# Kernel optimization log

Hardware: AMD Instinct MI355X
Metric: run time of the kernel (lower is better)

Reference implementation:

```python
import jax, jax.numpy as jnp
import numpy as np

B, N, H, OUT, T = 8192, 82, 10, 5, 3  # batch, n_nodes, hidden, output_channel, time_step


def setup_inputs() -> dict:
    key = jax.random.key(0)
    ks = jax.random.split(key, 20)

    def lin(kw, kb, fin, fout):
        w = jax.random.normal(kw, (fout, fin), jnp.float32) * (1.0 / np.sqrt(fin))
        b = jax.random.normal(kb, (fout,), jnp.float32) * 0.01
        return w, b

    w3w, b3w = lin(ks[0], ks[1], 2 * H, H)
    w3u, b3u = lin(ks[2], ks[3], H, H)
    w4w, b4w = lin(ks[4], ks[5], 2 * H, H)
    w5w, b5w = lin(ks[6], ks[7], 2 * H, H)
    w5u, b5u = lin(ks[8], ks[9], H, H)
    wout, bout = lin(ks[10], ks[11], 2 * H, OUT)
    return {
        'x': jax.random.normal(ks[12], (B, N, H), jnp.float32),
        'in_adj': jax.random.uniform(ks[13], (N, N), jnp.float32),
        'out_adj': jax.random.uniform(ks[14], (N, N), jnp.float32),
        'w3w': w3w, 'b3w': b3w, 'w3u': w3u, 'b3u': b3u,
        'w4w': w4w, 'b4w': b4w, 'w5w': w5w, 'b5w': b5w,
        'w5u': w5u, 'b5u': b5u, 'wout': wout, 'bout': bout,
    }


def _dense(v, w, b):
    return v @ w.T + b


def reference(x, in_adj, out_adj, w3w, b3w, w3u, b3u, w4w, b4w,
              w5w, b5w, w5u, b5u, wout, bout):
    b, n, h = x.shape
    nodes = x  # [B, N, H]
    fn = nodes.reshape(b * n, h)
    for _ in range(T):
        # neighbor aggregation; adjacency shared across batch (torch tiles it with repeat)
        a_in = jnp.einsum('ij,bjh->bih', in_adj, nodes)
        a_out = jnp.einsum('ij,bjh->bih', out_adj, nodes)
        av = jnp.concatenate([a_in, a_out], axis=-1).reshape(b * n, 2 * h)
        fn = nodes.reshape(b * n, h)
        zv = jax.nn.sigmoid(_dense(av, w3w, b3w) + _dense(fn, w3u, b3u))
        # NOTE: original torch code (bug) reuses fc_eq3_u here instead of fc_eq4_u
        rv = jax.nn.sigmoid(_dense(av, w4w, b4w) + _dense(fn, w3u, b3u))
        hv = jnp.tanh(_dense(av, w5w, b5w) + _dense(rv * fn, w5u, b5u))
        fn = (1.0 - zv) * fn + zv * hv
        nodes = fn.reshape(b, n, h)
    out_in = jnp.concatenate([fn, x.reshape(b * n, h)], axis=1)
    output = jnp.tanh(_dense(out_in, wout, bout))
    return output, fn
```

## Files before the change

kernel.cpp:

```cpp
#include <hip/hip_runtime.h>
#include <math.h>

#define B_TOTAL 8192
#define NN      82
#define HH      10
#define OUTC    5
#define TSTEP   3
#define BPB     3
#define THREADS 256
#define ROWP    12

__device__ __forceinline__ float sigmoid_(float x) {
    return 1.0f / (1.0f + __expf(-x));
}
__device__ __forceinline__ float tanh_(float x) {
    float e = __expf(2.0f * x);
    return 1.0f - 2.0f / (e + 1.0f);
}

__global__ void transpose_adj_kernel(const float* __restrict__ in_adj,
                                     const float* __restrict__ out_adj,
                                     float* __restrict__ adjT) {
    int idx = blockIdx.x * blockDim.x + threadIdx.x;
    if (idx < NN * NN) {
        int i = idx / NN;
        int j = idx - i * NN;
        adjT[j * NN + i]           = in_adj[i * NN + j];
        adjT[NN * NN + j * NN + i] = out_adj[i * NN + j];
    }
}

extern "C" __global__ __launch_bounds__(THREADS)
void ggnn_kernel(const float* __restrict__ x,
                 const float* __restrict__ adjT,
                 const float* __restrict__ w3w, const float* __restrict__ b3w,
                 const float* __restrict__ w3u, const float* __restrict__ b3u,
                 const float* __restrict__ w4w, const float* __restrict__ b4w,
                 const float* __restrict__ w5w, const float* __restrict__ b5w,
                 const float* __restrict__ w5u, const float* __restrict__ b5u,
                 const float* __restrict__ wout, const float* __restrict__ bout,
                 float* __restrict__ out0, float* __restrict__ out_fn)
{
    __shared__ __align__(16) float nodes[BPB][NN][ROWP];

    const int t     = threadIdx.x;
    const int bbase = blockIdx.x * BPB;
    const int bl    = t / NN;
    const int node  = t - bl * NN;
    const bool active = (bl < BPB) && (bbase + bl < B_TOTAL);
    const int b = bbase + bl;

    {
        int nb    = min(BPB, B_TOTAL - bbase);
        int nelem = nb * NN * HH;
        const float* src = x + (size_t)bbase * NN * HH;
        float* dst = &nodes[0][0][0];
        for (int k = t; k < nelem; k += THREADS) {
            int row = k / HH;
            int col = k - row * HH;
            dst[row * ROWP + col] = src[k];
        }
    }
    __syncthreads();

    float fn[HH];
    if (active) {
        #pragma unroll
        for (int h = 0; h < HH; ++h) fn[h] = nodes[bl][node][h];
    }

    const float* adjT_in  = adjT;
    const float* adjT_out = adjT + NN * NN;

    for (int step = 0; step < TSTEP; ++step) {
        float ai[HH], ao[HH];
        if (active) {
            #pragma unroll
            for (int h = 0; h < HH; ++h) { ai[h] = 0.0f; ao[h] = 0.0f; }

            const float* nrow = &nodes[bl][0][0];
            #pragma unroll 4
            for (int j = 0; j < NN; ++j) {
                float win = adjT_in [j * NN + node];
                float wot = adjT_out[j * NN + node];
                const float4* nj4 = reinterpret_cast<const float4*>(nrow + j * ROWP);
                float4 v0 = nj4[0];
                float4 v1 = nj4[1];
                float2 v2 = *reinterpret_cast<const float2*>(nrow + j * ROWP + 8);
                float v[HH] = {v0.x, v0.y, v0.z, v0.w, v1.x, v1.y, v1.z, v1.w, v2.x, v2.y};
                #pragma unroll
                for (int h = 0; h < HH; ++h) {
                    ai[h] = fmaf(win, v[h], ai[h]);
                    ao[h] = fmaf(wot, v[h], ao[h]);
                }
            }

            float av[2 * HH];
            #pragma unroll
            for (int h = 0; h < HH; ++h) { av[h] = ai[h]; av[HH + h] = ao[h]; }

            float u3[HH];
            #pragma unroll
            for (int h = 0; h < HH; ++h) {
                float s = b3u[h];
                #pragma unroll
                for (int k = 0; k < HH; ++k) s = fmaf(w3u[h * HH + k], fn[k], s);
                u3[h] = s;
            }

            float zv[HH], rv[HH];
            #pragma unroll
            for (int h = 0; h < HH; ++h) {
                float s1 = b3w[h];
                float s2 = b4w[h];
                #pragma unroll
                for (int k = 0; k < 2 * HH; ++k) {
                    s1 = fmaf(w3w[h * 2 * HH + k], av[k], s1);
                    s2 = fmaf(w4w[h * 2 * HH + k], av[k], s2);
                }
                zv[h] = sigmoid_(s1 + u3[h]);
                rv[h] = sigmoid_(s2 + u3[h]);
            }

            float rf[HH];
            #pragma unroll
            for (int k = 0; k < HH; ++k) rf[k] = rv[k] * fn[k];

            float hv[HH];
            #pragma unroll
            for (int h = 0; h < HH; ++h) {
                float s = b5w[h] + b5u[h];
                #pragma unroll
                for (int k = 0; k < 2 * HH; ++k) s = fmaf(w5w[h * 2 * HH + k], av[k], s);
                #pragma unroll
                for (int k = 0; k < HH; ++k)     s = fmaf(w5u[h * HH + k], rf[k], s);
                hv[h] = tanh_(s);
            }

            #pragma unroll
            for (int h = 0; h < HH; ++h) fn[h] = fn[h] + zv[h] * (hv[h] - fn[h]);
        }

        __syncthreads();
        if (active) {
            #pragma unroll
            for (int h = 0; h < HH; ++h) nodes[bl][node][h] = fn[h];
        }
        __syncthreads();
    }

    if (active) {
        size_t row = (size_t)b * NN + node;
        const float* xr = x + row * HH;
        float xi[HH];
        #pragma unroll
        for (int h = 0; h < HH; ++h) xi[h] = xr[h];

        #pragma unroll
        for (int c = 0; c < OUTC; ++c) {
            float s = bout[c];
            #pragma unroll
            for (int k = 0; k < HH; ++k) s = fmaf(wout[c * 2 * HH + k],      fn[k], s);
            #pragma unroll
            for (int k = 0; k < HH; ++k) s = fmaf(wout[c * 2 * HH + HH + k], xi[k], s);
            out0[row * OUTC + c] = tanh_(s);
        }
        #pragma unroll
        for (int h = 0; h < HH; ++h) out_fn[row * HH + h] = fn[h];
    }
}

extern "C" void kernel_launch(void* const* d_in, const int* in_sizes, int n_in,
                              void* d_out, int out_size, void* d_ws, size_t ws_size,
                              hipStream_t stream) {
    const float* x       = (const float*)d_in[0];
    const float* in_adj  = (const float*)d_in[1];
    const float* out_adj = (const float*)d_in[2];
    const float* w3w = (const float*)d_in[3];
    const float* b3w = (const float*)d_in[4];
    const float* w3u = (const float*)d_in[5];
    const float* b3u = (const float*)d_in[6];
    const float* w4w = (const float*)d_in[7];
    const float* b4w = (const float*)d_in[8];
    const float* w5w = (const float*)d_in[9];
    const float* b5w = (const float*)d_in[10];
    const float* w5u = (const float*)d_in[11];
    const float* b5u = (const float*)d_in[12];
    const float* wout = (const float*)d_in[13];
    const float* bout = (const float*)d_in[14];

    float* adjT = (float*)d_ws;
    float* out0 = (float*)d_out;
    float* out_fn = out0 + (size_t)B_TOTAL * NN * OUTC;

    transpose_adj_kernel<<<(NN * NN + 255) / 256, 256, 0, stream>>>(in_adj, out_adj, adjT);

    int grid = (B_TOTAL + BPB - 1) / BPB;
    ggnn_kernel<<<grid, THREADS, 0, stream>>>(
        x, adjT, w3w, b3w, w3u, b3u, w4w, b4w, w5w, b5w, w5u, b5u,
        wout, bout, out0, out_fn);
}
```

Measured before the change: 275.8 us.

## Process two batches per thread and interleave in/out adjacency as float2

Each thread now handles one node for two batch elements (6 batches per block instead of 3), so each adjacency weight loaded from global memory is reused across two batches. The in/out adjacency matrices are packed into a single interleaved float2 array, so one load fetches both weights. This halves the grid size and adjacency traffic per batch, but roughly doubles per-thread register pressure, which can reduce occupancy. Shared memory per block also doubles.

```diff
diff --git a/kernel.cpp b/kernel.cpp
--- a/kernel.cpp
+++ b/kernel.cpp
@@ -6,7 +6,9 @@
 #define HH      10
 #define OUTC    5
 #define TSTEP   3
-#define BPB     3
+#define GRP     3
+#define BPT     2
+#define BPB     (GRP * BPT)
 #define THREADS 256
 #define ROWP    12
 
@@ -20,19 +22,69 @@
 
 __global__ void transpose_adj_kernel(const float* __restrict__ in_adj,
                                      const float* __restrict__ out_adj,
-                                     float* __restrict__ adjT) {
+                                     float2* __restrict__ adjI) {
     int idx = blockIdx.x * blockDim.x + threadIdx.x;
     if (idx < NN * NN) {
         int i = idx / NN;
         int j = idx - i * NN;
-        adjT[j * NN + i]           = in_adj[i * NN + j];
-        adjT[NN * NN + j * NN + i] = out_adj[i * NN + j];
+        adjI[j * NN + i] = make_float2(in_adj[idx], out_adj[idx]);
+    }
+}
+
+__device__ __forceinline__ void gru_update(
+    float fn[HH], const float ai[HH], const float ao[HH],
+    const float* __restrict__ w3w, const float* __restrict__ b3w,
+    const float* __restrict__ w3u, const float* __restrict__ b3u,
+    const float* __restrict__ w4w, const float* __restrict__ b4w,
+    const float* __restrict__ w5w, const float* __restrict__ b5w,
+    const float* __restrict__ w5u, const float* __restrict__ b5u)
+{
+    float u3[HH];
+    #pragma unroll
+    for (int h = 0; h < HH; ++h) {
+        float s = b3u[h];
+        #pragma unroll
+        for (int k = 0; k < HH; ++k) s = fmaf(w3u[h * HH + k], fn[k], s);
+        u3[h] = s;
+    }
+
+    float zv[HH], rv[HH];
+    #pragma unroll
+    for (int h = 0; h < HH; ++h) {
+        float s1 = b3w[h];
+        float s2 = b4w[h];
+        #pragma unroll
+        for (int k = 0; k < HH; ++k) {
+            s1 = fmaf(w3w[h * 2 * HH + k],      ai[k], s1);
+            s1 = fmaf(w3w[h * 2 * HH + HH + k], ao[k], s1);
+            s2 = fmaf(w4w[h * 2 * HH + k],      ai[k], s2);
+            s2 = fmaf(w4w[h * 2 * HH + HH + k], ao[k], s2);
+        }
+        zv[h] = sigmoid_(s1 + u3[h]);
+        rv[h] = sigmoid_(s2 + u3[h]);
+    }
+
+    float rf[HH];
+    #pragma unroll
+    for (int k = 0; k < HH; ++k) rf[k] = rv[k] * fn[k];
+
+    #pragma unroll
+    for (int h = 0; h < HH; ++h) {
+        float s = b5w[h] + b5u[h];
+        #pragma unroll
+        for (int k = 0; k < HH; ++k) {
+            s = fmaf(w5w[h * 2 * HH + k],      ai[k], s);
+            s = fmaf(w5w[h * 2 * HH + HH + k], ao[k], s);
+            s = fmaf(w5u[h * HH + k],          rf[k], s);
+        }
+        float hv = tanh_(s);
+        fn[h] = fn[h] + zv[h] * (hv - fn[h]);
     }
 }
 
 extern "C" __global__ __launch_bounds__(THREADS)
 void ggnn_kernel(const float* __restrict__ x,
-                 const float* __restrict__ adjT,
+                 const float2* __restrict__ adjI,
                  const float* __restrict__ w3w, const float* __restrict__ b3w,
                  const float* __restrict__ w3u, const float* __restrict__ b3u,
                  const float* __restrict__ w4w, const float* __restrict__ b4w,
@@ -47,15 +99,18 @@
     const int bbase = blockIdx.x * BPB;
     const int bl    = t / NN;
     const int node  = t - bl * NN;
-    const bool active = (bl < BPB) && (bbase + bl < B_TOTAL);
-    const int b = bbase + bl;
+    const bool grp_ok = (bl < GRP);
+    const int b0 = bbase + bl;
+    const int b1 = bbase + bl + GRP;
+    const bool a0 = grp_ok && (b0 < B_TOTAL);
+    const bool a1 = grp_ok && (b1 < B_TOTAL);
 
     {
-        int nb    = min(BPB, B_TOTAL - bbase);
-        int nelem = nb * NN * HH;
-        const float* src = x + (size_t)bbase * NN * HH;
+        const size_t gbase = (size_t)bbase * NN * HH;
+        const int    limit = (int)min((size_t)(BPB * NN * HH), (size_t)B_TOTAL * NN * HH - gbase);
+        const float* src = x + gbase;
         float* dst = &nodes[0][0][0];
-        for (int k = t; k < nelem; k += THREADS) {
+        for (int k = t; k < limit; k += THREADS) {
             int row = k / HH;
             int col = k - row * HH;
             dst[row * ROWP + col] = src[k];
@@ -63,93 +118,69 @@
     }
     __syncthreads();
 
-    float fn[HH];
-    if (active) {
-        #pragma unroll
-        for (int h = 0; h < HH; ++h) fn[h] = nodes[bl][node][h];
-    }
-
-    const float* adjT_in  = adjT;
-    const float* adjT_out = adjT + NN * NN;
+    float fn0[HH], fn1[HH];
+    if (grp_ok) {
+        #pragma unroll
+        for (int h = 0; h < HH; ++h) {
+            fn0[h] = nodes[bl][node][h];
+            fn1[h] = nodes[bl + GRP][node][h];
+        }
+    }
 
     for (int step = 0; step < TSTEP; ++step) {
-        float ai[HH], ao[HH];
-        if (active) {
-            #pragma unroll
-            for (int h = 0; h < HH; ++h) { ai[h] = 0.0f; ao[h] = 0.0f; }
-
-            const float* nrow = &nodes[bl][0][0];
-            #pragma unroll 4
+        float ai0[HH], ao0[HH], ai1[HH], ao1[HH];
+        if (grp_ok) {
+            #pragma unroll
+            for (int h = 0; h < HH; ++h) {
+                ai0[h] = 0.0f; ao0[h] = 0.0f; ai1[h] = 0.0f; ao1[h] = 0.0f;
+            }
+
+            const float* n0 = &nodes[bl][0][0];
+            const float* n1 = &nodes[bl + GRP][0][0];
+            const float2* arow = adjI + node;
+
+            #pragma unroll 2
             for (int j = 0; j < NN; ++j) {
-                float win = adjT_in [j * NN + node];
-                float wot = adjT_out[j * NN + node];
-                const float4* nj4 = reinterpret_cast<const float4*>(nrow + j * ROWP);
-                float4 v0 = nj4[0];
-                float4 v1 = nj4[1];
-                float2 v2 = *reinterpret_cast<const float2*>(nrow + j * ROWP + 8);
-                float v[HH] = {v0.x, v0.y, v0.z, v0.w, v1.x, v1.y, v1.z, v1.w, v2.x, v2.y};
+                float2 w = arow[j * NN];
+                const float4* p0 = reinterpret_cast<const float4*>(n0 + j * ROWP);
+                const float4* p1 = reinterpret_cast<const float4*>(n1 + j * ROWP);
+                float4 v00 = p0[0], v01 = p0[1];
+                float2 v02 = *reinterpret_cast<const float2*>(n0 + j * ROWP + 8);
+                float4 v10 = p1[0], v11 = p1[1];
+                float2 v12 = *reinterpret_cast<const float2*>(n1 + j * ROWP + 8);
+                float v0[HH] = {v00.x, v00.y, v00.z, v00.w, v01.x, v01.y, v01.z, v01.w, v02.x, v02.y};
+                float v1[HH] = {v10.x, v10.y, v10.z, v10.w, v11.x, v11.y, v11.z, v11.w, v12.x, v12.y};
                 #pragma unroll
                 for (int h = 0; h < HH; ++h) {
-                    ai[h] = fmaf(win, v[h], ai[h]);
-                    ao[h] = fmaf(wot, v[h], ao[h]);
+                    ai0[h] = fmaf(w.x, v0[h], ai0[h]);
+                    ao0[h] = fmaf(w.y, v0[h], ao0[h]);
+                    ai1[h] = fmaf(w.x, v1[h], ai1[h]);
+                    ao1[h] = fmaf(w.y, v1[h], ao1[h]);
                 }
             }
 
-            float av[2 * HH];
-            #pragma unroll
-            for (int h = 0; h < HH; ++h) { av[h] = ai[h]; av[HH + h] = ao[h]; }
-
-            float u3[HH];
+            gru_update(fn0, ai0, ao0, w3w, b3w, w3u, b3u, w4w, b4w, w5w, b5w, w5u, b5u);
+            gru_update(fn1, ai1, ao1, w3w, b3w, w3u, b3u, w4w, b4w, w5w, b5w, w5u, b5u);
+        }
+
+        __syncthreads();
+        if (grp_ok) {
             #pragma unroll
             for (int h = 0; h < HH; ++h) {
-                float s = b3u[h];
-                #pragma unroll
-                for (int k = 0; k < HH; ++k) s = fmaf(w3u[h * HH + k], fn[k], s);
-                u3[h] = s;
+                nodes[bl][node][h]       = fn0[h];
+                nodes[bl + GRP][node][h] = fn1[h];
             }
-
-            float zv[HH], rv[HH];
-            #pragma unroll
-            for (int h = 0; h < HH; ++h) {
-                float s1 = b3w[h];
-                float s2 = b4w[h];
-                #pragma unroll
-                for (int k = 0; k < 2 * HH; ++k) {
-                    s1 = fmaf(w3w[h * 2 * HH + k], av[k], s1);
-                    s2 = fmaf(w4w[h * 2 * HH + k], av[k], s2);
-                }
-                zv[h] = sigmoid_(s1 + u3[h]);
-                rv[h] = sigmoid_(s2 + u3[h]);
-            }
-
-            float rf[HH];
-            #pragma unroll
-            for (int k = 0; k < HH; ++k) rf[k] = rv[k] * fn[k];
-
-            float hv[HH];
-            #pragma unroll
-            for (int h = 0; h < HH; ++h) {
-                float s = b5w[h] + b5u[h];
-                #pragma unroll
-                for (int k = 0; k < 2 * HH; ++k) s = fmaf(w5w[h * 2 * HH + k], av[k], s);
-                #pragma unroll
-                for (int k = 0; k < HH; ++k)     s = fmaf(w5u[h * HH + k], rf[k], s);
-                hv[h] = tanh_(s);
-            }
-
-            #pragma unroll
-            for (int h = 0; h < HH; ++h) fn[h] = fn[h] + zv[h] * (hv[h] - fn[h]);
-        }
-
+        }
         __syncthreads();
-        if (active) {
-            #pragma unroll
-            for (int h = 0; h < HH; ++h) nodes[bl][node][h] = fn[h];
-        }
-        __syncthreads();
-    }
-
-    if (active) {
+    }
+
+    #pragma unroll
+    for (int s = 0; s < BPT; ++s) {
+        const bool act = (s == 0) ? a0 : a1;
+        if (!act) continue;
+        const int b = (s == 0) ? b0 : b1;
+        const float* fn = (s == 0) ? fn0 : fn1;
+
         size_t row = (size_t)b * NN + node;
         const float* xr = x + row * HH;
         float xi[HH];
@@ -158,12 +189,12 @@
 
         #pragma unroll
         for (int c = 0; c < OUTC; ++c) {
-            float s = bout[c];
-            #pragma unroll
-            for (int k = 0; k < HH; ++k) s = fmaf(wout[c * 2 * HH + k],      fn[k], s);
-            #pragma unroll
-            for (int k = 0; k < HH; ++k) s = fmaf(wout[c * 2 * HH + HH + k], xi[k], s);
-            out0[row * OUTC + c] = tanh_(s);
+            float s2 = bout[c];
+            #pragma unroll
+            for (int k = 0; k < HH; ++k) s2 = fmaf(wout[c * 2 * HH + k],      fn[k], s2);
+            #pragma unroll
+            for (int k = 0; k < HH; ++k) s2 = fmaf(wout[c * 2 * HH + HH + k], xi[k], s2);
+            out0[row * OUTC + c] = tanh_(s2);
         }
         #pragma unroll
         for (int h = 0; h < HH; ++h) out_fn[row * HH + h] = fn[h];
@@ -189,14 +220,14 @@
     const float* wout = (const float*)d_in[13];
     const float* bout = (const float*)d_in[14];
 
-    float* adjT = (float*)d_ws;
+    float2* adjI = (float2*)d_ws;
     float* out0 = (float*)d_out;
     float* out_fn = out0 + (size_t)B_TOTAL * NN * OUTC;
 
-    transpose_adj_kernel<<<(NN * NN + 255) / 256, 256, 0, stream>>>(in_adj, out_adj, adjT);
+    transpose_adj_kernel<<<(NN * NN + 255) / 256, 256, 0, stream>>>(in_adj, out_adj, adjI);
 
     int grid = (B_TOTAL + BPB - 1) / BPB;
     ggnn_kernel<<<grid, THREADS, 0, stream>>>(
-        x, adjT, w3w, b3w, w3u, b3u, w4w, b4w, w5w, b5w, w5u, b5u,
+        x, adjI, w3w, b3w, w3u, b3u, w4w, b4w, w5w, b5w, w5u, b5u,
         wout, bout, out0, out_fn);
 }
```

New measurement: 305.5 us. 10.8% more time.
